# Kernel tuning notes

Measured on AMD Instinct MI355X. Metric: run time of the kernel, lower is better.

## Reference

```python
import jax, jax.numpy as jnp
import numpy as np

N, E = 50000, 800000
F_NODE, F_EDGE, H, LAT, MAXN = 128, 16, 128, 64, 200


def setup_inputs() -> dict:
    key = jax.random.key(0)
    ks = jax.random.split(key, 40)
    s = 0.05
    p = {
        'x': jax.random.normal(ks[0], (N, F_NODE), jnp.float32),
        'edge_index': jax.random.randint(ks[1], (2, E), 0, N, jnp.int64),
        'edge_attr': jax.random.normal(ks[2], (E, F_EDGE), jnp.float32),
        'eps': jax.random.normal(ks[3], (1, LAT), jnp.float32),
        'num_nodes': N,
        # GATConv layer 1 (heads=1)
        'W1': jax.random.normal(ks[4], (F_NODE, H), jnp.float32) * s,
        'att_src1': jax.random.normal(ks[5], (H,), jnp.float32) * s,
        'att_dst1': jax.random.normal(ks[6], (H,), jnp.float32) * s,
        'We1': jax.random.normal(ks[7], (F_EDGE, H), jnp.float32) * s,
        'att_e1': jax.random.normal(ks[8], (H,), jnp.float32) * s,
        'b1': jnp.zeros((H,), jnp.float32),
        # GATConv layer 2
        'W2': jax.random.normal(ks[9], (H, H), jnp.float32) * s,
        'att_src2': jax.random.normal(ks[10], (H,), jnp.float32) * s,
        'att_dst2': jax.random.normal(ks[11], (H,), jnp.float32) * s,
        'We2': jax.random.normal(ks[12], (F_EDGE, H), jnp.float32) * s,
        'att_e2': jax.random.normal(ks[13], (H,), jnp.float32) * s,
        'b2': jnp.zeros((H,), jnp.float32),
        # heads
        'mu_W': jax.random.normal(ks[14], (H, LAT), jnp.float32) * s,
        'mu_b': jnp.zeros((LAT,), jnp.float32),
        'lv_W': jax.random.normal(ks[15], (H, LAT), jnp.float32) * s,
        'lv_b': jnp.zeros((LAT,), jnp.float32),
        'dec_W': jax.random.normal(ks[16], (LAT, H), jnp.float32) * s,
        'dec_b': jnp.zeros((H,), jnp.float32),
        'adj_W1': jax.random.normal(ks[17], (H, H), jnp.float32) * s,
        'adj_b1': jnp.zeros((H,), jnp.float32),
        'adj_W2': jax.random.normal(ks[18], (H, MAXN), jnp.float32) * s,
        'adj_b2': jnp.zeros((MAXN,), jnp.float32),
        'nd_W1': jax.random.normal(ks[19], (H, H), jnp.float32) * s,
        'nd_b1': jnp.zeros((H,), jnp.float32),
        'nd_W2': jax.random.normal(ks[20], (H, F_NODE), jnp.float32) * s,
        'nd_b2': jnp.zeros((F_NODE,), jnp.float32),
    }
    return p


def _gat(h, src, dst, ea, W, a_s, a_d, We, a_e, b, n):
    # PyG GATConv, heads=1: linear transform, per-edge attention, segment softmax over dst
    g = h @ W                                     # [n, H]
    alpha = jax.nn.leaky_relu((g @ a_s)[src] + (g @ a_d)[dst] + (ea @ We) @ a_e,
                              negative_slope=0.2)  # [E']
    m = jax.ops.segment_max(alpha, dst, num_segments=n)
    ex = jnp.exp(alpha - m[dst])
    den = jax.ops.segment_sum(ex, dst, num_segments=n)
    w = ex / den[dst]
    return jax.ops.segment_sum(w[:, None] * g[src], dst, num_segments=n) + b


def _forward(x, edge_index, edge_attr, eps, num_nodes,
             W1, att_src1, att_dst1, We1, att_e1, b1,
             W2, att_src2, att_dst2, We2, att_e2, b2,
             mu_W, mu_b, lv_W, lv_b, dec_W, dec_b,
             adj_W1, adj_b1, adj_W2, adj_b2, nd_W1, nd_b1, nd_W2, nd_b2):
    n = x.shape[0]
    src, dst = edge_index[0], edge_index[1]
    # add self loops; self-loop edge_attr = per-node mean of incoming edge_attr (PyG fill_value='mean')
    deg = jax.ops.segment_sum(jnp.ones((src.shape[0],), x.dtype), dst, num_segments=n)
    mean_ea = jax.ops.segment_sum(edge_attr, dst, num_segments=n) / jnp.maximum(deg, 1.0)[:, None]
    loop = jnp.arange(n)
    src_f = jnp.concatenate([src, loop])
    dst_f = jnp.concatenate([dst, loop])
    ea_f = jnp.concatenate([edge_attr, mean_ea])
    h = jax.nn.relu(_gat(x, src_f, dst_f, ea_f, W1, att_src1, att_dst1, We1, att_e1, b1, n))
    h = jax.nn.relu(_gat(h, src_f, dst_f, ea_f, W2, att_src2, att_dst2, We2, att_e2, b2, n))
    hg = h.mean(axis=0, keepdims=True)            # global_mean_pool, single graph -> [1, H]
    mu = hg @ mu_W + mu_b
    logvar = hg @ lv_W + lv_b
    z = mu + eps * jnp.exp(0.5 * logvar)
    hd = jax.nn.relu(z @ dec_W + dec_b)           # [1, H]
    hn = jnp.broadcast_to(hd[:, None, :], (1, num_nodes, hd.shape[-1]))
    adj = jax.nn.relu(hn @ adj_W1 + adj_b1) @ adj_W2 + adj_b2   # [1, n, MAXN]
    adj = adj[:, :, :num_nodes]
    nodes = jax.nn.relu(hn @ nd_W1 + nd_b1) @ nd_W2 + nd_b2     # [1, n, F_NODE]
    return adj, nodes, mu, logvar


def reference(x, edge_index, edge_attr, eps, num_nodes,
              W1, att_src1, att_dst1, We1, att_e1, b1,
              W2, att_src2, att_dst2, We2, att_e2, b2,
              mu_W, mu_b, lv_W, lv_b, dec_W, dec_b,
              adj_W1, adj_b1, adj_W2, adj_b2, nd_W1, nd_b1, nd_W2, nd_b2):
    return _forward(x, edge_index, edge_attr, eps, num_nodes,
                    W1, att_src1, att_dst1, We1, att_e1, b1,
                    W2, att_src2, att_dst2, We2, att_e2, b2,
                    mu_W, mu_b, lv_W, lv_b, dec_W, dec_b,
                    adj_W1, adj_b1, adj_W2, adj_b2, nd_W1, nd_b1, nd_W2, nd_b2)
```

## Files before the change

### kernel.cpp

```cpp
#include <hip/hip_runtime.h>
#include <math.h>

#define NN   50000
#define EE   800000
#define EF   850000
#define HH   128
#define FE   16
#define LATD 64
#define MAXNN 200

#define ADJ_TOT   10000000
#define NODES_TOT 6400000
#define OUT_TOT   16400000
#define MU_OFF    16400000
#define LV_OFF    16400064

#define SCATBLOCKS 3125
#define GEMMBLOCKS 782

typedef __attribute__((ext_vector_type(8))) short bf16x8;
typedef __attribute__((ext_vector_type(4))) float f32x4;
typedef __attribute__((ext_vector_type(2))) float f32x2;

__device__ __forceinline__ unsigned short f2bf(float f){
  unsigned int u = __float_as_uint(f);
  unsigned int r = (u + 0x7FFFu + ((u>>16)&1u)) >> 16;
  return (unsigned short)r;
}
__device__ __forceinline__ float bf2f(unsigned short h){
  return __uint_as_float(((unsigned int)h)<<16);
}

__global__ __launch_bounds__(256) void kdegsetup(const int* __restrict__ ei, int* ideg,
                       unsigned short* __restrict__ erank,
                       const float* We1, const float* ae1, const float* We2, const float* ae2,
                       float* wa1, float* wa2,
                       const float* W1, const float* W2,
                       unsigned short* Wp1, unsigned short* Wp2){
  int i = blockIdx.x*256 + threadIdx.x;
  if(i < EE) erank[i] = (unsigned short)atomicAdd(&ideg[ei[EE+i]], 1);
  if(i < FE){
    float s1=0.f, s2=0.f;
    for(int j=0;j<HH;j++){ s1 += We1[i*HH+j]*ae1[j]; s2 += We2[i*HH+j]*ae2[j]; }
    wa1[i]=s1; wa2[i]=s2;
  }
  if(i < HH*HH){
    int n = i >> 7, k = i & 127;
    Wp1[i] = f2bf(W1[k*HH + n]);
    Wp2[i] = f2bf(W2[k*HH + n]);
  }
}

__global__ void kscan1(const int* __restrict__ ideg, int* rowstart, int* blocksum){
  __shared__ int sd[1024];
  int t=threadIdx.x; int i=blockIdx.x*1024+t;
  int v = (i<NN)? (ideg[i]+1) : 0;
  sd[t]=v; __syncthreads();
  for(int off=1; off<1024; off<<=1){
    int x = (t>=off)? sd[t-off] : 0;
    __syncthreads();
    sd[t] += x;
    __syncthreads();
  }
  if(i<NN) rowstart[i] = sd[t]-v;
  if(t==1023) blocksum[blockIdx.x]=sd[1023];
}
__global__ void kscan2(const int* __restrict__ blocksum, int* __restrict__ blockoff, int nb){
  int t = threadIdx.x;
  int v = (t<nb)? blocksum[t] : 0;
  int inc = v;
  #pragma unroll
  for(int off=1; off<64; off<<=1){
    int x = __shfl_up(inc, off);
    if(t>=off) inc += x;
  }
  if(t<=nb) blockoff[t] = inc - v;
}
__global__ void kscan3(int* rowstart, const int* __restrict__ blockoff, int nb){
  int i=blockIdx.x*blockDim.x+threadIdx.x;
  if(i<NN) rowstart[i]+=blockoff[i>>10];
  if(i==0) rowstart[NN]=blockoff[nb];
}

__device__ __forceinline__ void scatter_body(int e,
                         const int* __restrict__ ei, const float* __restrict__ ea,
                         const float* __restrict__ wa1, const float* __restrict__ wa2,
                         const int* __restrict__ rowstart, const unsigned short* __restrict__ erank,
                         uint2* __restrict__ csr){
  if(e>=EE) return;
  int s=ei[e], d=ei[EE+e];
  const float4* ea4 = (const float4*)(ea + (size_t)e*FE);
  float4 v0=ea4[0], v1=ea4[1], v2=ea4[2], v3=ea4[3];
  float va[16]={v0.x,v0.y,v0.z,v0.w, v1.x,v1.y,v1.z,v1.w,
                v2.x,v2.y,v2.z,v2.w, v3.x,v3.y,v3.z,v3.w};
  float d1=0.f,d2=0.f;
  #pragma unroll
  for(int f=0;f<FE;f++){ d1+=va[f]*wa1[f]; d2+=va[f]*wa2[f]; }
  int pos = rowstart[d] + (int)erank[e];
  uint2 en; en.x = (unsigned)s;
  en.y = (unsigned)f2bf(d1) | ((unsigned)f2bf(d2)<<16);
  csr[pos] = en;
}

__device__ __forceinline__ void gemm_body(int bid, int tid, const void* __restrict__ hin, int h_is_fp32,
    const unsigned short* __restrict__ Wp,
    const float* __restrict__ atts, const float* __restrict__ attd,
    unsigned char* __restrict__ A8, float* __restrict__ asrc, float* __restrict__ adst){
  int lane = tid & 63;
  int wid  = tid >> 6;
  int l = lane & 15, q = lane >> 4;
  int r0 = bid*64 + wid*16;
  if(r0 >= NN) return;
  const unsigned short* hb = (const unsigned short*)hin;
  const float*          hf = (const float*)hin;
  int row = r0 + l;

  f32x4 acc[8];
  #pragma unroll
  for(int t=0;t<8;t++) acc[t]=(f32x4){0.f,0.f,0.f,0.f};

  #pragma unroll
  for(int kb=0;kb<4;kb++){
    bf16x8 a;
    if(h_is_fp32){
      const float* p = hf + (size_t)row*HH + kb*32 + q*8;
      float4 u0 = *(const float4*)(p);
      float4 u1 = *(const float4*)(p+4);
      a[0]=(short)f2bf(u0.x); a[1]=(short)f2bf(u0.y); a[2]=(short)f2bf(u0.z); a[3]=(short)f2bf(u0.w);
      a[4]=(short)f2bf(u1.x); a[5]=(short)f2bf(u1.y); a[6]=(short)f2bf(u1.z); a[7]=(short)f2bf(u1.w);
    } else {
      a = *(const bf16x8*)(hb + (size_t)row*HH + kb*32 + q*8);
    }
    #pragma unroll
    for(int t=0;t<8;t++){
      bf16x8 b = *(const bf16x8*)(Wp + (size_t)(t*16+l)*HH + kb*32 + q*8);
      acc[t] = __builtin_amdgcn_mfma_f32_16x16x32_bf16(a, b, acc[t], 0,0,0);
    }
  }

  float av[8], dv[8];
  #pragma unroll
  for(int t=0;t<8;t++){ av[t]=atts[t*16+l]; dv[t]=attd[t*16+l]; }
  #pragma unroll
  for(int reg=0;reg<4;reg++){
    float ps=0.f, pd=0.f;
    #pragma unroll
    for(int t=0;t<8;t++){ ps+=acc[t][reg]*av[t]; pd+=acc[t][reg]*dv[t]; }
    #pragma unroll
    for(int m=8;m>=1;m>>=1){ ps+=__shfl_xor(ps,m,16); pd+=__shfl_xor(pd,m,16); }
    if(l==0){ int R=r0+q*4+reg; asrc[R]=ps; adst[R]=pd; }
  }
  #pragma unroll
  for(int t=0;t<8;t++)
    #pragma unroll
    for(int reg=0;reg<4;reg++){
      int pk = __builtin_amdgcn_cvt_pk_fp8_f32(acc[t][reg], 0.f, 0, false);
      A8[(size_t)(r0+q*4+reg)*HH + t*16 + l] = (unsigned char)(pk & 0xFF);
    }
}

__global__ __launch_bounds__(256) void kgemm3(const void* __restrict__ hin, int h_is_fp32,
    const unsigned short* __restrict__ Wp,
    const float* __restrict__ atts, const float* __restrict__ attd,
    unsigned char* __restrict__ A8, float* __restrict__ asrc, float* __restrict__ adst){
  gemm_body(blockIdx.x, threadIdx.x, hin, h_is_fp32, Wp, atts, attd, A8, asrc, adst);
}

__global__ __launch_bounds__(256) void kscatgemm(
    const int* __restrict__ ei, const float* __restrict__ ea,
    const float* __restrict__ wa1, const float* __restrict__ wa2,
    const int* __restrict__ rowstart, const unsigned short* __restrict__ erank,
    uint2* __restrict__ csr,
    const void* __restrict__ hin, int h_is_fp32,
    const unsigned short* __restrict__ Wp,
    const float* __restrict__ atts, const float* __restrict__ attd,
    unsigned char* __restrict__ A8, float* __restrict__ asrc, float* __restrict__ adst){
  if(blockIdx.x < SCATBLOCKS){
    scatter_body(blockIdx.x*256 + threadIdx.x, ei, ea, wa1, wa2, rowstart, erank, csr);
  } else {
    gemm_body(blockIdx.x - SCATBLOCKS, threadIdx.x, hin, h_is_fp32, Wp, atts, attd, A8, asrc, adst);
  }
}

__global__ __launch_bounds__(256) void kgat(const unsigned char* __restrict__ A8,
    const float* __restrict__ asrc, const float* __restrict__ adst,
    const int* __restrict__ rowstart, const uint2* __restrict__ csr,
    int etsel, const float* __restrict__ bias,
    float* __restrict__ alphabuf, int* __restrict__ srcbuf,
    unsigned short* __restrict__ Bout){
  int lane = threadIdx.x & 63;
  int wid  = threadIdx.x >> 6;
  int i = blockIdx.x*4 + wid;
  if(i >= NN) return;
  int base = rowstart[i];
  int len  = rowstart[i+1]-base;
  float adi = adst[i];
  int lq = lane & 15;
  int qq = lane >> 4;
  float av[8];
  #pragma unroll
  for(int j=0;j<8;j++) av[j]=0.f;

  if(__builtin_expect(len <= 64, 1)){
    int s = i; float et = 0.f;
    if(lane < len-1){
      uint2 en = csr[base+lane];
      s = (int)en.x;
      et = etsel ? bf2f((unsigned short)(en.y>>16)) : bf2f((unsigned short)(en.y & 0xFFFFu));
    }
    float ets = (lane < len-1) ? et : 0.f;
    #pragma unroll
    for(int mk=32;mk>=1;mk>>=1) ets += __shfl_xor(ets,mk);
    if(lane == len-1) et = ets / fmaxf((float)(len-1), 1.f);
    float a = -1e30f;
    if(lane < len){
      a = asrc[s] + adi + et;
      a = fmaxf(a, 0.2f*a);
    }
    float m = a;
    #pragma unroll
    for(int mk=32;mk>=1;mk>>=1) m = fmaxf(m, __shfl_xor(m,mk));
    float ex = (lane<len) ? __expf(a-m) : 0.f;
    float sm = ex;
    #pragma unroll
    for(int mk=32;mk>=1;mk>>=1) sm += __shfl_xor(sm,mk);
    ex *= __builtin_amdgcn_rcpf(sm);

    int P4 = (len+3)>>2;
    for(int t0=0; t0<P4; t0+=6){
      int skv[6]; float w[6];
      #pragma unroll
      for(int j=0;j<6;j++){
        if(t0+j < P4){
          int idx = 4*(t0+j) + qq;
          skv[j] = __shfl(s, idx);
          w[j]   = __shfl(ex, idx);
        } else { skv[j] = i; w[j] = 0.f; }
      }
      unsigned ux[6], uy[6];
      #pragma unroll
      for(int j=0;j<6;j++){
        uint2 u = *(const uint2*)(A8 + (size_t)skv[j]*HH + lq*8);
        ux[j]=u.x; uy[j]=u.y;
      }
      #pragma unroll
      for(int j=0;j<6;j++){
        f32x2 v;
        v=__builtin_amdgcn_cvt_pk_f32_fp8((int)ux[j],false); av[0]+=w[j]*v[0]; av[1]+=w[j]*v[1];
        v=__builtin_amdgcn_cvt_pk_f32_fp8((int)ux[j],true ); av[2]+=w[j]*v[0]; av[3]+=w[j]*v[1];
        v=__builtin_amdgcn_cvt_pk_f32_fp8((int)uy[j],false); av[4]+=w[j]*v[0]; av[5]+=w[j]*v[1];
        v=__builtin_amdgcn_cvt_pk_f32_fp8((int)uy[j],true ); av[6]+=w[j]*v[0]; av[7]+=w[j]*v[1];
      }
    }
  } else {
    int deg = len-1;
    float lm = -1e30f, ets = 0.f;
    for(int k=lane;k<deg;k+=64){
      uint2 en = csr[base+k];
      int sr = (int)en.x;
      float et = etsel ? bf2f((unsigned short)(en.y>>16)) : bf2f((unsigned short)(en.y & 0xFFFFu));
      ets += et;
      float a = asrc[sr] + adi + et;
      a = fmaxf(a, 0.2f*a);
      alphabuf[base+k]=a; srcbuf[base+k]=sr;
      lm = fmaxf(lm,a);
    }
    #pragma unroll
    for(int mk=32;mk>=1;mk>>=1){
      ets += __shfl_xor(ets,mk);
      lm   = fmaxf(lm, __shfl_xor(lm,mk));
    }
    float aself = asrc[i] + adi + ets/(float)deg;
    aself = fmaxf(aself, 0.2f*aself);
    lm = fmaxf(lm, aself);
    float ls=0.f;
    for(int k=lane;k<len;k+=64){
      float a = (k<deg)? alphabuf[base+k] : aself;
      float e_ = __expf(a-lm);
      alphabuf[base+k]=e_;
      ls += e_;
    }
    #pragma unroll
    for(int mk=32;mk>=1;mk>>=1) ls += __shfl_xor(ls,mk);
    float inv = 1.f/ls;
    int P4 = (len+3)>>2;
    for(int t=0;t<P4;t++){
      int k = 4*t + qq;
      int sk = i; float wk = 0.f;
      if(k<len){
        sk = (k<deg)? srcbuf[base+k] : i;
        wk = alphabuf[base+k]*inv;
      }
      uint2 u = *(const uint2*)(A8 + (size_t)sk*HH + lq*8);
      f32x2 v;
      v=__builtin_amdgcn_cvt_pk_f32_fp8((int)u.x,false); av[0]+=wk*v[0]; av[1]+=wk*v[1];
      v=__builtin_amdgcn_cvt_pk_f32_fp8((int)u.x,true ); av[2]+=wk*v[0]; av[3]+=wk*v[1];
      v=__builtin_amdgcn_cvt_pk_f32_fp8((int)u.y,false); av[4]+=wk*v[0]; av[5]+=wk*v[1];
      v=__builtin_amdgcn_cvt_pk_f32_fp8((int)u.y,true ); av[6]+=wk*v[0]; av[7]+=wk*v[1];
    }
  }

  #pragma unroll
  for(int j=0;j<8;j++){
    av[j] += __shfl_xor(av[j],16);
    av[j] += __shfl_xor(av[j],32);
  }
  if(qq==0){
    const float4* bp = (const float4*)(bias + lq*8);
    float4 b0=bp[0], b1=bp[1];
    float o0=fmaxf(av[0]+b0.x,0.f), o1=fmaxf(av[1]+b0.y,0.f);
    float o2=fmaxf(av[2]+b0.z,0.f), o3=fmaxf(av[3]+b0.w,0.f);
    float o4=fmaxf(av[4]+b1.x,0.f), o5=fmaxf(av[5]+b1.y,0.f);
    float o6=fmaxf(av[6]+b1.z,0.f), o7=fmaxf(av[7]+b1.w,0.f);
    uint4 ov;
    ov.x=(unsigned)f2bf(o0)|((unsigned)f2bf(o1)<<16);
    ov.y=(unsigned)f2bf(o2)|((unsigned)f2bf(o3)<<16);
    ov.z=(unsigned)f2bf(o4)|((unsigned)f2bf(o5)<<16);
    ov.w=(unsigned)f2bf(o6)|((unsigned)f2bf(o7)<<16);
    *(uint4*)(Bout + (size_t)i*HH + lq*8) = ov;
  }
}

__global__ __launch_bounds__(256) void khg(const unsigned short* __restrict__ B, float* hgsum){
  int f = threadIdx.x & 127;
  int half = threadIdx.x >> 7;
  float s=0.f;
  for(int i = blockIdx.x*2+half; i < NN; i += gridDim.x*2)
    s += bf2f(B[(size_t)i*HH + f]);
  __shared__ float sd[256];
  sd[threadIdx.x]=s; __syncthreads();
  if(half==0) atomicAdd(&hgsum[f], sd[threadIdx.x]+sd[threadIdx.x+128]);
}

__global__ __launch_bounds__(256) void kdec(const float* __restrict__ hgsum, const float* __restrict__ eps,
   const float* muW,const float* mub,const float* lvW,const float* lvb,
   const float* decW,const float* decb,
   const float* aW1,const float* ab1,const float* aW2,const float* ab2,
   const float* nW1,const float* nb1,const float* nW2,const float* nb2,
   float* out, float* rowadj, float* rownodes){
  __shared__ float hg[HH], z[LATD], hd[HH], t1[HH], t2[HH];
  int t=threadIdx.x;
  if(t<HH) hg[t]=hgsum[t]*(1.0f/NN);
  __syncthreads();
  if(t<LATD){
    float mu=mub[t], lv=lvb[t];
    #pragma unroll 8
    for(int k=0;k<HH;k++){ mu += hg[k]*muW[k*LATD+t]; lv += hg[k]*lvW[k*LATD+t]; }
    out[MU_OFF+t]=mu; out[LV_OFF+t]=lv;
    z[t]=mu + eps[t]*expf(0.5f*lv);
  }
  __syncthreads();
  if(t<HH){
    float a=decb[t];
    #pragma unroll 8
    for(int k=0;k<LATD;k++) a += z[k]*decW[k*HH+t];
    hd[t]=fmaxf(a,0.f);
  }
  __syncthreads();
  if(t<HH){
    float a=ab1[t];
    #pragma unroll 8
    for(int k=0;k<HH;k++) a += hd[k]*aW1[k*HH+t];
    t1[t]=fmaxf(a,0.f);
  } else {
    int j=t-HH;
    float a=nb1[j];
    #pragma unroll 8
    for(int k=0;k<HH;k++) a += hd[k]*nW1[k*HH+j];
    t2[j]=fmaxf(a,0.f);
  }
  __syncthreads();
  for(int j=t;j<MAXNN;j+=256){
    float a=ab2[j];
    #pragma unroll 8
    for(int k=0;k<HH;k++) a += t1[k]*aW2[k*MAXNN+j];
    rowadj[j]=a;
  }
  if(t<HH){
    float a=nb2[t];
    #pragma unroll 8
    for(int k=0;k<HH;k++) a += t2[k]*nW2[k*HH+t];
    rownodes[t]=a;
  }
}

__global__ __launch_bounds__(256) void kbcast(const float* __restrict__ rowadj,
                                              const float* __restrict__ rownodes,
                                              float* __restrict__ out){
  __shared__ float row[MAXNN+HH];
  int t=threadIdx.x;
  if(t<MAXNN) row[t]=rowadj[t];
  if(t<HH) row[MAXNN+t]=rownodes[t];
  __syncthreads();
  int stride=gridDim.x*blockDim.x;
  const int tot4 = OUT_TOT/4;
  for(int q=blockIdx.x*blockDim.x+t; q<tot4; q+=stride){
    int idx = q*4;
    float4 vv;
    if(idx<ADJ_TOT){
      int j = idx % MAXNN;
      vv = *(const float4*)&row[j];
    } else {
      int j = (idx-ADJ_TOT) & (HH-1);
      vv = *(const float4*)&row[MAXNN+j];
    }
    *(float4*)&out[idx] = vv;
  }
}

extern "C" void kernel_launch(void* const* d_in, const int* in_sizes, int n_in,
                              void* d_out, int out_size, void* d_ws, size_t ws_size,
                              hipStream_t stream){
  const float* x   = (const float*)d_in[0];
  const int*   ei  = (const int*)d_in[1];
  const float* ea  = (const float*)d_in[2];
  const float* eps = (const float*)d_in[3];
  const float* W1  =(const float*)d_in[5];
  const float* as1 =(const float*)d_in[6];
  const float* ad1 =(const float*)d_in[7];
  const float* We1 =(const float*)d_in[8];
  const float* ae1 =(const float*)d_in[9];
  const float* b1  =(const float*)d_in[10];
  const float* W2  =(const float*)d_in[11];
  const float* as2 =(const float*)d_in[12];
  const float* ad2 =(const float*)d_in[13];
  const float* We2 =(const float*)d_in[14];
  const float* ae2 =(const float*)d_in[15];
  const float* b2  =(const float*)d_in[16];
  const float* muW =(const float*)d_in[17];
  const float* mub =(const float*)d_in[18];
  const float* lvW =(const float*)d_in[19];
  const float* lvb =(const float*)d_in[20];
  const float* decW=(const float*)d_in[21];
  const float* decb=(const float*)d_in[22];
  const float* aW1 =(const float*)d_in[23];
  const float* ab1 =(const float*)d_in[24];
  const float* aW2 =(const float*)d_in[25];
  const float* ab2 =(const float*)d_in[26];
  const float* nW1 =(const float*)d_in[27];
  const float* nb1 =(const float*)d_in[28];
  const float* nW2 =(const float*)d_in[29];
  const float* nb2 =(const float*)d_in[30];
  float* out=(float*)d_out;

  char* w=(char*)d_ws;
  unsigned char*  A8  = (unsigned char*)w;  w += (size_t)NN*HH;
  unsigned short* Bbf = (unsigned short*)w; w += (size_t)NN*HH*2;
  unsigned short* Wp1 = (unsigned short*)w; w += (size_t)HH*HH*2;
  unsigned short* Wp2 = (unsigned short*)w; w += (size_t)HH*HH*2;
  uint2*  csr      = (uint2*)w;  w += (size_t)EF*8;
  float*  alphabuf = (float*)w;  w += (size_t)EF*4;
  int*    srcbuf   = (int*)w;    w += (size_t)EF*4;
  unsigned short* erank = (unsigned short*)w; w += (size_t)EE*2;
  int*    rowstart = (int*)w;    w += (size_t)(NN+1)*4;
  int*    ideg     = (int*)w;    w += (size_t)NN*4;
  float*  hgsum    = (float*)w;  w += 128*4;
  float*  asrc     = (float*)w;  w += (size_t)NN*4;
  float*  adst     = (float*)w;  w += (size_t)NN*4;
  float*  wa1      = (float*)w;  w += 16*4;
  float*  wa2      = (float*)w;  w += 16*4;
  float*  rowadj   = (float*)w;  w += 256*4;
  float*  rownodes = (float*)w;  w += 128*4;
  int*    blocksum = (int*)w;    w += 64*4;
  int*    blockoff = (int*)w;    w += 64*4;

  int nb = (NN+1023)/1024;
  int gatblocks  = (NN+3)/4;

  hipMemsetAsync(ideg, 0, (size_t)(NN+128)*4, stream);
  hipLaunchKernelGGL(kdegsetup, dim3((EE+255)/256), dim3(256), 0, stream,
                     ei, ideg, erank, We1, ae1, We2, ae2, wa1, wa2, W1, W2, Wp1, Wp2);
  hipLaunchKernelGGL(kscan1, dim3(nb), dim3(1024), 0, stream, ideg, rowstart, blocksum);
  hipLaunchKernelGGL(kscan2, dim3(1), dim3(64), 0, stream, blocksum, blockoff, nb);
  hipLaunchKernelGGL(kscan3, dim3((NN+255)/256), dim3(256), 0, stream, rowstart, blockoff, nb);
  hipLaunchKernelGGL(kscatgemm, dim3(SCATBLOCKS+GEMMBLOCKS), dim3(256), 0, stream,
                     ei, ea, wa1, wa2, rowstart, erank, csr,
                     (const void*)x, 1, Wp1, as1, ad1, A8, asrc, adst);
  hipLaunchKernelGGL(kgat,  dim3(gatblocks), dim3(256), 0, stream,
                     A8, asrc, adst, rowstart, csr, 0, b1, alphabuf, srcbuf, Bbf);
  hipLaunchKernelGGL(kgemm3, dim3(GEMMBLOCKS), dim3(256), 0, stream,
                     (const void*)Bbf, 0, Wp2, as2, ad2, A8, asrc, adst);
  hipLaunchKernelGGL(kgat,  dim3(gatblocks), dim3(256), 0, stream,
                     A8, asrc, adst, rowstart, csr, 1, b2, alphabuf, srcbuf, Bbf);
  hipLaunchKernelGGL(khg,   dim3(512), dim3(256), 0, stream, Bbf, hgsum);
  hipLaunchKernelGGL(kdec,  dim3(1), dim3(256), 0, stream, hgsum, eps,
                     muW,mub,lvW,lvb,decW,decb,aW1,ab1,aW2,ab2,nW1,nb1,nW2,nb2,
                     out, rowadj, rownodes);
  hipLaunchKernelGGL(kbcast, dim3(2048), dim3(256), 0, stream, rowadj, rownodes, out);
}
```

Measured before the change: 411.1 us.

## Reschedule graph preprocessing, fuse scan kernels, fold mean-pool into second GAT

Replaces the memset with a small prep kernel that zeroes the degree and pool buffers. The layer-1 GEMM now overlaps with the degree-counting atomics instead of the CSR scatter. The two scan-offset kernels merge into one, and the scatter runs as its own kernel with two edges per thread. The separate mean-pool kernel is removed: the second GAT pass atomically accumulates its outputs into 64 striped partial-sum slots, which the decoder reduces. This cuts launches and a full re-read of the hidden matrix, at the cost of extra atomics in the GAT kernel.

```diff
diff --git a/kernel.cpp b/kernel.cpp
--- a/kernel.cpp
+++ b/kernel.cpp
@@ -15,8 +15,9 @@
 #define MU_OFF    16400000
 #define LV_OFF    16400064
 
-#define SCATBLOCKS 3125
 #define GEMMBLOCKS 782
+#define DEGBLOCKS  3125
+#define HGSLOTS    64
 
 typedef __attribute__((ext_vector_type(8))) short bf16x8;
 typedef __attribute__((ext_vector_type(4))) float f32x4;
@@ -31,14 +32,14 @@
   return __uint_as_float(((unsigned int)h)<<16);
 }
 
-__global__ __launch_bounds__(256) void kdegsetup(const int* __restrict__ ei, int* ideg,
-                       unsigned short* __restrict__ erank,
+__global__ __launch_bounds__(256) void kprep(int* ideg, float* hgpart,
                        const float* We1, const float* ae1, const float* We2, const float* ae2,
                        float* wa1, float* wa2,
                        const float* W1, const float* W2,
                        unsigned short* Wp1, unsigned short* Wp2){
   int i = blockIdx.x*256 + threadIdx.x;
-  if(i < EE) erank[i] = (unsigned short)atomicAdd(&ideg[ei[EE+i]], 1);
+  if(i < NN) ideg[i]=0;
+  if(i < HGSLOTS*HH) hgpart[i]=0.f;
   if(i < FE){
     float s1=0.f, s2=0.f;
     for(int j=0;j<HH;j++){ s1 += We1[i*HH+j]*ae1[j]; s2 += We2[i*HH+j]*ae2[j]; }
@@ -49,57 +50,6 @@
     Wp1[i] = f2bf(W1[k*HH + n]);
     Wp2[i] = f2bf(W2[k*HH + n]);
   }
-}
-
-__global__ void kscan1(const int* __restrict__ ideg, int* rowstart, int* blocksum){
-  __shared__ int sd[1024];
-  int t=threadIdx.x; int i=blockIdx.x*1024+t;
-  int v = (i<NN)? (ideg[i]+1) : 0;
-  sd[t]=v; __syncthreads();
-  for(int off=1; off<1024; off<<=1){
-    int x = (t>=off)? sd[t-off] : 0;
-    __syncthreads();
-    sd[t] += x;
-    __syncthreads();
-  }
-  if(i<NN) rowstart[i] = sd[t]-v;
-  if(t==1023) blocksum[blockIdx.x]=sd[1023];
-}
-__global__ void kscan2(const int* __restrict__ blocksum, int* __restrict__ blockoff, int nb){
-  int t = threadIdx.x;
-  int v = (t<nb)? blocksum[t] : 0;
-  int inc = v;
-  #pragma unroll
-  for(int off=1; off<64; off<<=1){
-    int x = __shfl_up(inc, off);
-    if(t>=off) inc += x;
-  }
-  if(t<=nb) blockoff[t] = inc - v;
-}
-__global__ void kscan3(int* rowstart, const int* __restrict__ blockoff, int nb){
-  int i=blockIdx.x*blockDim.x+threadIdx.x;
-  if(i<NN) rowstart[i]+=blockoff[i>>10];
-  if(i==0) rowstart[NN]=blockoff[nb];
-}
-
-__device__ __forceinline__ void scatter_body(int e,
-                         const int* __restrict__ ei, const float* __restrict__ ea,
-                         const float* __restrict__ wa1, const float* __restrict__ wa2,
-                         const int* __restrict__ rowstart, const unsigned short* __restrict__ erank,
-                         uint2* __restrict__ csr){
-  if(e>=EE) return;
-  int s=ei[e], d=ei[EE+e];
-  const float4* ea4 = (const float4*)(ea + (size_t)e*FE);
-  float4 v0=ea4[0], v1=ea4[1], v2=ea4[2], v3=ea4[3];
-  float va[16]={v0.x,v0.y,v0.z,v0.w, v1.x,v1.y,v1.z,v1.w,
-                v2.x,v2.y,v2.z,v2.w, v3.x,v3.y,v3.z,v3.w};
-  float d1=0.f,d2=0.f;
-  #pragma unroll
-  for(int f=0;f<FE;f++){ d1+=va[f]*wa1[f]; d2+=va[f]*wa2[f]; }
-  int pos = rowstart[d] + (int)erank[e];
-  uint2 en; en.x = (unsigned)s;
-  en.y = (unsigned)f2bf(d1) | ((unsigned)f2bf(d2)<<16);
-  csr[pos] = en;
 }
 
 __device__ __forceinline__ void gemm_body(int bid, int tid, const void* __restrict__ hin, int h_is_fp32,
@@ -166,20 +116,79 @@
   gemm_body(blockIdx.x, threadIdx.x, hin, h_is_fp32, Wp, atts, attd, A8, asrc, adst);
 }
 
-__global__ __launch_bounds__(256) void kscatgemm(
-    const int* __restrict__ ei, const float* __restrict__ ea,
-    const float* __restrict__ wa1, const float* __restrict__ wa2,
-    const int* __restrict__ rowstart, const unsigned short* __restrict__ erank,
-    uint2* __restrict__ csr,
+__global__ __launch_bounds__(256) void kdeggemm(
+    const int* __restrict__ ei, int* ideg, unsigned short* __restrict__ erank,
     const void* __restrict__ hin, int h_is_fp32,
     const unsigned short* __restrict__ Wp,
     const float* __restrict__ atts, const float* __restrict__ attd,
     unsigned char* __restrict__ A8, float* __restrict__ asrc, float* __restrict__ adst){
-  if(blockIdx.x < SCATBLOCKS){
-    scatter_body(blockIdx.x*256 + threadIdx.x, ei, ea, wa1, wa2, rowstart, erank, csr);
+  if(blockIdx.x < GEMMBLOCKS){
+    gemm_body(blockIdx.x, threadIdx.x, hin, h_is_fp32, Wp, atts, attd, A8, asrc, adst);
   } else {
-    gemm_body(blockIdx.x - SCATBLOCKS, threadIdx.x, hin, h_is_fp32, Wp, atts, attd, A8, asrc, adst);
-  }
+    int e = (blockIdx.x - GEMMBLOCKS)*256 + threadIdx.x;
+    if(e < EE) erank[e] = (unsigned short)atomicAdd(&ideg[ei[EE+e]], 1);
+  }
+}
+
+__global__ void kscan1(const int* __restrict__ ideg, int* rowstart, int* blocksum){
+  __shared__ int sd[1024];
+  int t=threadIdx.x; int i=blockIdx.x*1024+t;
+  int v = (i<NN)? (ideg[i]+1) : 0;
+  sd[t]=v; __syncthreads();
+  for(int off=1; off<1024; off<<=1){
+    int x = (t>=off)? sd[t-off] : 0;
+    __syncthreads();
+    sd[t] += x;
+    __syncthreads();
+  }
+  if(i<NN) rowstart[i] = sd[t]-v;
+  if(t==1023) blocksum[blockIdx.x]=sd[1023];
+}
+__global__ __launch_bounds__(256) void kscan3i(int* rowstart, const int* __restrict__ blocksum, int nb){
+  __shared__ int bo[64];
+  int t = threadIdx.x;
+  if(t < 64){
+    int v = (t<nb)? blocksum[t] : 0;
+    int inc = v;
+    #pragma unroll
+    for(int off=1; off<64; off<<=1){
+      int x = __shfl_up(inc, off);
+      if(t>=off) inc += x;
+    }
+    bo[t] = inc - v;
+  }
+  __syncthreads();
+  int i = blockIdx.x*256 + t;
+  if(i<NN) rowstart[i] += bo[i>>10];
+  if(i==0) rowstart[NN] = bo[nb];
+}
+
+__device__ __forceinline__ unsigned etpack(const float4* a4,
+                         const float* __restrict__ wa1, const float* __restrict__ wa2){
+  float4 v0=a4[0], v1=a4[1], v2=a4[2], v3=a4[3];
+  float va[16]={v0.x,v0.y,v0.z,v0.w, v1.x,v1.y,v1.z,v1.w,
+                v2.x,v2.y,v2.z,v2.w, v3.x,v3.y,v3.z,v3.w};
+  float d1=0.f,d2=0.f;
+  #pragma unroll
+  for(int f=0;f<FE;f++){ d1+=va[f]*wa1[f]; d2+=va[f]*wa2[f]; }
+  return (unsigned)f2bf(d1) | ((unsigned)f2bf(d2)<<16);
+}
+__global__ __launch_bounds__(256) void kscatter(const int* __restrict__ ei, const float* __restrict__ ea,
+                         const float* __restrict__ wa1, const float* __restrict__ wa2,
+                         const int* __restrict__ rowstart, const unsigned short* __restrict__ erank,
+                         uint2* __restrict__ csr){
+  int e0 = (blockIdx.x*256 + threadIdx.x)*2;
+  if(e0>=EE) return;
+  int sA=ei[e0],    sB=ei[e0+1];
+  int dA=ei[EE+e0], dB=ei[EE+e0+1];
+  int rA=(int)erank[e0], rB=(int)erank[e0+1];
+  int pA=rowstart[dA]+rA, pB=rowstart[dB]+rB;
+  const float4* a4 = (const float4*)(ea + (size_t)e0*FE);
+  unsigned yA = etpack(a4,   wa1, wa2);
+  unsigned yB = etpack(a4+4, wa1, wa2);
+  uint2 enA; enA.x=(unsigned)sA; enA.y=yA;
+  uint2 enB; enB.x=(unsigned)sB; enB.y=yB;
+  csr[pA]=enA; csr[pB]=enB;
 }
 
 __global__ __launch_bounds__(256) void kgat(const unsigned char* __restrict__ A8,
@@ -187,7 +196,7 @@
     const int* __restrict__ rowstart, const uint2* __restrict__ csr,
     int etsel, const float* __restrict__ bias,
     float* __restrict__ alphabuf, int* __restrict__ srcbuf,
-    unsigned short* __restrict__ Bout){
+    unsigned short* __restrict__ Bout, float* __restrict__ hgpart){
   int lane = threadIdx.x & 63;
   int wid  = threadIdx.x >> 6;
   int i = blockIdx.x*4 + wid;
@@ -318,21 +327,15 @@
     ov.z=(unsigned)f2bf(o4)|((unsigned)f2bf(o5)<<16);
     ov.w=(unsigned)f2bf(o6)|((unsigned)f2bf(o7)<<16);
     *(uint4*)(Bout + (size_t)i*HH + lq*8) = ov;
-  }
-}
-
-__global__ __launch_bounds__(256) void khg(const unsigned short* __restrict__ B, float* hgsum){
-  int f = threadIdx.x & 127;
-  int half = threadIdx.x >> 7;
-  float s=0.f;
-  for(int i = blockIdx.x*2+half; i < NN; i += gridDim.x*2)
-    s += bf2f(B[(size_t)i*HH + f]);
-  __shared__ float sd[256];
-  sd[threadIdx.x]=s; __syncthreads();
-  if(half==0) atomicAdd(&hgsum[f], sd[threadIdx.x]+sd[threadIdx.x+128]);
-}
-
-__global__ __launch_bounds__(256) void kdec(const float* __restrict__ hgsum, const float* __restrict__ eps,
+    if(etsel){
+      float* hp = hgpart + (size_t)(blockIdx.x & (HGSLOTS-1))*HH + lq*8;
+      atomicAdd(hp+0,o0); atomicAdd(hp+1,o1); atomicAdd(hp+2,o2); atomicAdd(hp+3,o3);
+      atomicAdd(hp+4,o4); atomicAdd(hp+5,o5); atomicAdd(hp+6,o6); atomicAdd(hp+7,o7);
+    }
+  }
+}
+
+__global__ __launch_bounds__(256) void kdec(const float* __restrict__ hgpart, const float* __restrict__ eps,
    const float* muW,const float* mub,const float* lvW,const float* lvb,
    const float* decW,const float* decb,
    const float* aW1,const float* ab1,const float* aW2,const float* ab2,
@@ -340,7 +343,12 @@
    float* out, float* rowadj, float* rownodes){
   __shared__ float hg[HH], z[LATD], hd[HH], t1[HH], t2[HH];
   int t=threadIdx.x;
-  if(t<HH) hg[t]=hgsum[t]*(1.0f/NN);
+  if(t<HH){
+    float s=0.f;
+    #pragma unroll 8
+    for(int k=0;k<HGSLOTS;k++) s += hgpart[k*HH+t];
+    hg[t]=s*(1.0f/NN);
+  }
   __syncthreads();
   if(t<LATD){
     float mu=mub[t], lv=lvb[t];
@@ -454,7 +462,7 @@
   unsigned short* erank = (unsigned short*)w; w += (size_t)EE*2;
   int*    rowstart = (int*)w;    w += (size_t)(NN+1)*4;
   int*    ideg     = (int*)w;    w += (size_t)NN*4;
-  float*  hgsum    = (float*)w;  w += 128*4;
+  float*  hgpart   = (float*)w;  w += (size_t)HGSLOTS*HH*4;
   float*  asrc     = (float*)w;  w += (size_t)NN*4;
   float*  adst     = (float*)w;  w += (size_t)NN*4;
   float*  wa1      = (float*)w;  w += 16*4;
@@ -462,28 +470,26 @@
   float*  rowadj   = (float*)w;  w += 256*4;
   float*  rownodes = (float*)w;  w += 128*4;
   int*    blocksum = (int*)w;    w += 64*4;
-  int*    blockoff = (int*)w;    w += 64*4;
 
   int nb = (NN+1023)/1024;
   int gatblocks  = (NN+3)/4;
 
-  hipMemsetAsync(ideg, 0, (size_t)(NN+128)*4, stream);
-  hipLaunchKernelGGL(kdegsetup, dim3((EE+255)/256), dim3(256), 0, stream,
-                     ei, ideg, erank, We1, ae1, We2, ae2, wa1, wa2, W1, W2, Wp1, Wp2);
+  hipLaunchKernelGGL(kprep, dim3((NN+255)/256), dim3(256), 0, stream,
+                     ideg, hgpart, We1, ae1, We2, ae2, wa1, wa2, W1, W2, Wp1, Wp2);
+  hipLaunchKernelGGL(kdeggemm, dim3(GEMMBLOCKS+DEGBLOCKS), dim3(256), 0, stream,
+                     ei, ideg, erank,
+                     (const void*)x, 1, Wp1, as1, ad1, A8, asrc, adst);
   hipLaunchKernelGGL(kscan1, dim3(nb), dim3(1024), 0, stream, ideg, rowstart, blocksum);
-  hipLaunchKernelGGL(kscan2, dim3(1), dim3(64), 0, stream, blocksum, blockoff, nb);
-  hipLaunchKernelGGL(kscan3, dim3((NN+255)/256), dim3(256), 0, stream, rowstart, blockoff, nb);
-  hipLaunchKernelGGL(kscatgemm, dim3(SCATBLOCKS+GEMMBLOCKS), dim3(256), 0, stream,
-                     ei, ea, wa1, wa2, rowstart, erank, csr,
-                     (const void*)x, 1, Wp1, as1, ad1, A8, asrc, adst);
+  hipLaunchKernelGGL(kscan3i, dim3((NN+255)/256), dim3(256), 0, stream, rowstart, blocksum, nb);
+  hipLaunchKernelGGL(kscatter, dim3((EE/2+255)/256), dim3(256), 0, stream,
+                     ei, ea, wa1, wa2, rowstart, erank, csr);
   hipLaunchKernelGGL(kgat,  dim3(gatblocks), dim3(256), 0, stream,
-                     A8, asrc, adst, rowstart, csr, 0, b1, alphabuf, srcbuf, Bbf);
+                     A8, asrc, adst, rowstart, csr, 0, b1, alphabuf, srcbuf, Bbf, hgpart);
   hipLaunchKernelGGL(kgemm3, dim3(GEMMBLOCKS), dim3(256), 0, stream,
                      (const void*)Bbf, 0, Wp2, as2, ad2, A8, asrc, adst);
   hipLaunchKernelGGL(kgat,  dim3(gatblocks), dim3(256), 0, stream,
-                     A8, asrc, adst, rowstart, csr, 1, b2, alphabuf, srcbuf, Bbf);
-  hipLaunchKernelGGL(khg,   dim3(512), dim3(256), 0, stream, Bbf, hgsum);
-  hipLaunchKernelGGL(kdec,  dim3(1), dim3(256), 0, stream, hgsum, eps,
+                     A8, asrc, adst, rowstart, csr, 1, b2, alphabuf, srcbuf, Bbf, hgpart);
+  hipLaunchKernelGGL(kdec,  dim3(1), dim3(256), 0, stream, hgpart, eps,
                      muW,mub,lvW,lvb,decW,decb,aW1,ab1,aW2,ab2,nW1,nb1,nW2,nb2,
                      out, rowadj, rownodes);
   hipLaunchKernelGGL(kbcast, dim3(2048), dim3(256), 0, stream, rowadj, rownodes, out);
```

Result: slower. 578.9 us (+40.8%).
